# Performance work log

Measured on AMD Instinct MI355X. Metric: run time of the kernel, lower is better.

## Reference

```python
import jax, jax.numpy as jnp
import numpy as np

HID = 64
CTX = 64
STEPS = 2
RANK = 16
NODES = 1024
B, T = 16, 24
EPS = 1e-5


def _linear(x, W, b):
    # torch nn.Linear: x @ W.T + b, W is [out, in]
    return jnp.einsum('...i,oi->...o', x, W) + b


def _gelu(x):
    return jax.nn.gelu(x, approximate=False)


def _diffusion(adj, state, Ws, bs):
    # Ws: [S, out, in], bs: [S, out]
    term = jnp.zeros_like(state)
    for s in range(Ws.shape[0]):
        state = jnp.einsum('nm,btmf->btnf', adj, state)
        term = term + _linear(state, Ws[s], bs[s])
    return term


def setup_inputs() -> dict:
    key = jax.random.key(0)
    ks = jax.random.split(key, 32)
    f32 = jnp.float32
    def w(k, *shape, scale=None):
        s = scale if scale is not None else 1.0 / np.sqrt(shape[-1])
        return jax.random.uniform(k, shape, f32, -s, s)
    inp = {
        'x': jax.random.normal(ks[0], (B, T, NODES, HID), f32),
        'a_fwd': jax.random.uniform(ks[1], (NODES, NODES), f32),
        'context': jax.random.normal(ks[2], (B, T, NODES, CTX), f32),
        'W_self': w(ks[3], HID, HID), 'b_self': w(ks[4], HID),
        'W_fwd': w(ks[5], STEPS, HID, HID), 'b_fwd': w(ks[6], STEPS, HID),
        'W_bwd': w(ks[7], STEPS, HID, HID), 'b_bwd': w(ks[8], STEPS, HID),
        'W_adp': w(ks[9], STEPS, HID, HID), 'b_adp': w(ks[10], STEPS, HID),
        'Wg1': w(ks[11], HID, CTX), 'bg1': w(ks[12], HID),
        'Wg2': w(ks[13], 4, HID), 'bg2': w(ks[14], 4),
        'Ws1': w(ks[15], HID, CTX), 'bs1': w(ks[16], HID),
        'Ws2': w(ks[17], HID, HID), 'bs2': w(ks[18], HID),
        'W_src': w(ks[19], 1, CTX), 'b_src': w(ks[20], 1),
        'W_dst': w(ks[21], 1, CTX), 'b_dst': w(ks[22], 1),
        'emb_src': jax.random.normal(ks[23], (NODES, RANK), f32) * 0.02,
        'emb_dst': jax.random.normal(ks[24], (NODES, RANK), f32) * 0.02,
        'gamma': jnp.ones((HID,), f32), 'beta': jnp.zeros((HID,), f32),
    }
    return inp


def reference(x, a_fwd, context, W_self, b_self, W_fwd, b_fwd, W_bwd, b_bwd,
              W_adp, b_adp, Wg1, bg1, Wg2, bg2, Ws1, bs1, Ws2, bs2,
              W_src, b_src, W_dst, b_dst, emb_src, emb_dst, gamma, beta):
    a_bwd = a_fwd.T
    # adaptive adjacency: softmax(relu(Es @ Ed^T)) over last dim
    a_adp = jax.nn.softmax(jax.nn.relu(emb_src @ emb_dst.T), axis=-1)

    gates = jax.nn.sigmoid(_linear(_gelu(_linear(context, Wg1, bg1)), Wg2, bg2))  # [b,t,n,4]
    scale = jax.nn.sigmoid(_linear(_gelu(_linear(context, Ws1, bs1)), Ws2, bs2))  # [b,t,n,F]
    src_gate = jax.nn.sigmoid(_linear(context, W_src, b_src))  # [b,t,n,1]
    dst_gate = jax.nn.sigmoid(_linear(context, W_dst, b_dst))  # [b,t,n,1]

    self_term = _linear(x, W_self, b_self)
    fwd_term = _diffusion(a_fwd, x * dst_gate, W_fwd, b_fwd)
    bwd_term = _diffusion(a_bwd, x * src_gate, W_bwd, b_bwd)
    adp_term = _diffusion(a_adp, x, W_adp, b_adp)

    mixed = (gates[..., 0:1] * self_term + gates[..., 1:2] * fwd_term
             + gates[..., 2:3] * bwd_term + gates[..., 3:4] * adp_term) * scale

    h = x + _gelu(mixed)  # dropout is identity in eval mode
    mu = jnp.mean(h, axis=-1, keepdims=True)
    var = jnp.mean(jnp.square(h - mu), axis=-1, keepdims=True)
    return (h - mu) * jax.lax.rsqrt(var + EPS) * gamma + beta
```

## Files before the change

### kernel.cpp

```cpp
#include <hip/hip_runtime.h>
#include <math.h>

typedef unsigned short u16;
typedef short short8 __attribute__((ext_vector_type(8)));
typedef float f32x4 __attribute__((ext_vector_type(4)));

#define LN_EPS 1e-5f

__device__ __forceinline__ float gelu_exact(float x){
    return 0.5f * x * (1.0f + erff(x * 0.70710678118654752f));
}
__device__ __forceinline__ float sigmoidf_(float x){
    return 1.0f / (1.0f + __expf(-x));
}
__device__ __forceinline__ u16 f2bf(float f){
    unsigned u = __float_as_uint(f);
    u += 0x7fffu + ((u >> 16) & 1u);
    return (u16)(u >> 16);
}
__device__ __forceinline__ float b2f(u16 u){
    return __uint_as_float(((unsigned)u) << 16);
}

#define GLLDS(gp, lp) __builtin_amdgcn_global_load_lds( \
    (const __attribute__((address_space(1))) unsigned int*)(const void*)(gp), \
    (__attribute__((address_space(3))) unsigned int*)(void*)(lp), 16, 0, 0)

__global__ __launch_bounds__(256) void k_adp(const float* __restrict__ es,
                                             const float* __restrict__ ed,
                                             u16* __restrict__ aadp){
    __shared__ float srow[1024];
    __shared__ float s_es[16];
    __shared__ float sredm[4];
    __shared__ float sreds[4];
    const int n   = blockIdx.x;
    const int tid = threadIdx.x;
    const int wid = tid >> 6, lane = tid & 63;
    if (tid < 16) s_es[tid] = es[n*16 + tid];
    __syncthreads();
    float lmax = 0.0f;
    for (int m = tid; m < 1024; m += 256){
        const float* edm = ed + m*16;
        float z = 0.f;
        #pragma unroll
        for (int r = 0; r < 16; r++) z = fmaf(s_es[r], edm[r], z);
        z = fmaxf(z, 0.0f);
        srow[m] = z;
        lmax = fmaxf(lmax, z);
    }
    #pragma unroll
    for (int o = 32; o > 0; o >>= 1) lmax = fmaxf(lmax, __shfl_xor(lmax, o, 64));
    if (lane == 0) sredm[wid] = lmax;
    __syncthreads();
    const float tmax = fmaxf(fmaxf(sredm[0], sredm[1]), fmaxf(sredm[2], sredm[3]));
    float lsum = 0.f;
    for (int m = tid; m < 1024; m += 256){
        float e = expf(srow[m] - tmax);
        srow[m] = e;
        lsum += e;
    }
    #pragma unroll
    for (int o = 32; o > 0; o >>= 1) lsum += __shfl_xor(lsum, o, 64);
    if (lane == 0) sreds[wid] = lsum;
    __syncthreads();
    const float inv = 1.0f / (sreds[0] + sreds[1] + sreds[2] + sreds[3]);
    for (int m = tid; m < 1024; m += 256) aadp[(size_t)n*1024 + m] = f2bf(srow[m] * inv);
}

__global__ __launch_bounds__(256) void k_cvtbwd(const float* __restrict__ a,
                                                u16* __restrict__ afwd,
                                                u16* __restrict__ abwd){
    __shared__ float t[32][33];
    const int bx = blockIdx.x*32, by = blockIdx.y*32;
    const int tx = threadIdx.x & 31, ty = threadIdx.x >> 5;
    #pragma unroll
    for (int i = 0; i < 4; i++){
        const float v = a[(size_t)(by + ty + 8*i)*1024 + bx + tx];
        t[ty + 8*i][tx] = v;
        afwd[(size_t)(by + ty + 8*i)*1024 + bx + tx] = f2bf(v);
    }
    __syncthreads();
    #pragma unroll
    for (int i = 0; i < 4; i++)
        abwd[(size_t)(bx + ty + 8*i)*1024 + by + tx] = f2bf(t[tx][ty + 8*i]);
}

__global__ __launch_bounds__(256, 4) void k_gating(
    const float* __restrict__ x,    const float* __restrict__ ctx,
    const float* __restrict__ Wg1,  const float* __restrict__ bg1,
    const float* __restrict__ Wg2,  const float* __restrict__ bg2,
    const float* __restrict__ Ws1,  const float* __restrict__ bs1,
    const float* __restrict__ Ws2,  const float* __restrict__ bs2,
    const float* __restrict__ Wsrc, const float* __restrict__ bsrc,
    const float* __restrict__ Wdst, const float* __restrict__ bdst,
    const float* __restrict__ Wself,const float* __restrict__ bself,
    float* __restrict__ gates, u16* __restrict__ scaleb,
    float* __restrict__ acc,
    u16* __restrict__ xTp, u16* __restrict__ xTd, u16* __restrict__ xTs)
{
    __shared__ u16 H1[8192];
    __shared__ u16 H2[8192];
    __shared__ float sgate[128], dgate[128];

    const int tid  = threadIdx.x;
    const int wv   = tid >> 6, lane = tid & 63;
    const int lr   = lane & 15, lg = lane >> 4;
    const int wtok = wv * 32;
    const int tokbase = blockIdx.x * 128;
    const int bt = blockIdx.x >> 3;
    const int n0 = (blockIdx.x & 7) * 128;

    auto stage_coop = [&](u16* H, const float* g){
        #pragma unroll
        for (int i = 0; i < 8; i++){
            const int fid = i*256 + tid;
            const int t = fid >> 4, q = fid & 15;
            const float4 v = *(const float4*)&g[(size_t)t*64 + q*4];
            ushort4 s;
            s.x = f2bf(v.x); s.y = f2bf(v.y); s.z = f2bf(v.z); s.w = f2bf(v.w);
            *(ushort4*)&H[t*64 + ((((q>>1) ^ (t & 7)) << 3) | ((q & 1)*4))] = s;
        }
    };
    auto afrag = [&](const u16* H, int row, int kb)->short8{
        return *(const short8*)&H[wv*2048 + row*64 + ((kb ^ (row & 7)) << 3)];
    };
    auto wfrag = [&](const float* W, int o, int kb8)->short8{
        const float4 a = *(const float4*)&W[o*64 + kb8];
        const float4 b = *(const float4*)&W[o*64 + kb8 + 4];
        short8 s;
        s[0]=f2bf(a.x); s[1]=f2bf(a.y); s[2]=f2bf(a.z); s[3]=f2bf(a.w);
        s[4]=f2bf(b.x); s[5]=f2bf(b.y); s[6]=f2bf(b.z); s[7]=f2bf(b.w);
        return s;
    };
    auto gemm32 = [&](const u16* Hs, const float* W, const float* bias, f32x4 (&c)[2][4]){
        #pragma unroll
        for (int n = 0; n < 4; n++){
            const float bv = bias[n*16 + lr];
            #pragma unroll
            for (int m = 0; m < 2; m++){ f32x4 t = {bv,bv,bv,bv}; c[m][n] = t; }
        }
        #pragma unroll
        for (int kk = 0; kk < 2; kk++){
            short8 a[2];
            #pragma unroll
            for (int m = 0; m < 2; m++) a[m] = afrag(Hs, m*16 + lr, kk*4 + lg);
            #pragma unroll
            for (int n = 0; n < 4; n++){
                const short8 w = wfrag(W, n*16 + lr, kk*32 + lg*8);
                #pragma unroll
                for (int m = 0; m < 2; m++)
                    c[m][n] = __builtin_amdgcn_mfma_f32_16x16x32_bf16(a[m], w, c[m][n], 0,0,0);
            }
        }
    };
    auto storeH = [&](u16* Hd, f32x4 (&c)[2][4]){
        #pragma unroll
        for (int m = 0; m < 2; m++)
            #pragma unroll
            for (int n = 0; n < 4; n++){
                const int f = n*16 + lr;
                #pragma unroll
                for (int r = 0; r < 4; r++){
                    const int t = m*16 + lg*4 + r;
                    Hd[wv*2048 + t*64 + ((((f>>3) ^ (t & 7)) << 3) | (f & 7))] = f2bf(c[m][n][r]);
                }
            }
    };

    stage_coop(H1, ctx + (size_t)tokbase*64);
    __syncthreads();

    f32x4 c[2][4];

    gemm32(H1, Wg1, bg1, c);
    #pragma unroll
    for (int m = 0; m < 2; m++)
        #pragma unroll
        for (int n = 0; n < 4; n++)
            #pragma unroll
            for (int r = 0; r < 4; r++) c[m][n][r] = gelu_exact(c[m][n][r]);
    storeH(H2, c);

    {
        f32x4 c2[2];
        const float bv = (lr == 0) ? bsrc[0] : (lr == 1 ? bdst[0] : 0.f);
        #pragma unroll
        for (int m = 0; m < 2; m++){ f32x4 t = {bv,bv,bv,bv}; c2[m] = t; }
        #pragma unroll
        for (int kk = 0; kk < 2; kk++){
            short8 a[2];
            #pragma unroll
            for (int m = 0; m < 2; m++) a[m] = afrag(H1, m*16 + lr, kk*4 + lg);
            short8 w = {0,0,0,0,0,0,0,0};
            if (lr == 0) w = wfrag(Wsrc, 0, kk*32 + lg*8);
            else if (lr == 1) w = wfrag(Wdst, 0, kk*32 + lg*8);
            #pragma unroll
            for (int m = 0; m < 2; m++)
                c2[m] = __builtin_amdgcn_mfma_f32_16x16x32_bf16(a[m], w, c2[m], 0,0,0);
        }
        #pragma unroll
        for (int m = 0; m < 2; m++)
            #pragma unroll
            for (int r = 0; r < 4; r++){
                const int t = wtok + m*16 + lg*4 + r;
                const float v = sigmoidf_(c2[m][r]);
                if (lr == 0) sgate[t] = v;
                if (lr == 1) dgate[t] = v;
            }
    }

    gemm32(H1, Ws1, bs1, c);
    #pragma unroll
    for (int m = 0; m < 2; m++)
        #pragma unroll
        for (int n = 0; n < 4; n++)
            #pragma unroll
            for (int r = 0; r < 4; r++) c[m][n][r] = gelu_exact(c[m][n][r]);
    storeH(H1, c);

    float g0[2][4];
    {
        f32x4 c3[2];
        const float bv = (lr < 4) ? bg2[lr] : 0.f;
        #pragma unroll
        for (int m = 0; m < 2; m++){ f32x4 t = {bv,bv,bv,bv}; c3[m] = t; }
        #pragma unroll
        for (int kk = 0; kk < 2; kk++){
            short8 a[2];
            #pragma unroll
            for (int m = 0; m < 2; m++) a[m] = afrag(H2, m*16 + lr, kk*4 + lg);
            short8 w = {0,0,0,0,0,0,0,0};
            if (lr < 4) w = wfrag(Wg2, lr, kk*32 + lg*8);
            #pragma unroll
            for (int m = 0; m < 2; m++)
                c3[m] = __builtin_amdgcn_mfma_f32_16x16x32_bf16(a[m], w, c3[m], 0,0,0);
        }
        #pragma unroll
        for (int m = 0; m < 2; m++)
            #pragma unroll
            for (int r = 0; r < 4; r++){
                const float v = sigmoidf_(c3[m][r]);
                if (lr < 4)
                    gates[(size_t)(tokbase + wtok + m*16 + lg*4 + r)*4 + lr] = v;
                g0[m][r] = __shfl(v, lane & 48, 64);
            }
    }

    gemm32(H1, Ws2, bs2, c);
    #pragma unroll
    for (int m = 0; m < 2; m++)
        #pragma unroll
        for (int n = 0; n < 4; n++)
            #pragma unroll
            for (int r = 0; r < 4; r++) c[m][n][r] = sigmoidf_(c[m][n][r]);
    storeH(H1, c);
    {
        #pragma unroll
        for (int it = 0; it < 4; it++){
            const int r2  = wtok + it*8 + (lane >> 3);
            const int sub = lane & 7;
            const short8 v = *(const short8*)&H1[r2*64 + ((sub ^ (r2 & 7)) << 3)];
            *(short8*)&scaleb[(size_t)(tokbase + r2)*64 + sub*8] = v;
        }
    }

    __syncthreads();
    stage_coop(H2, x + (size_t)tokbase*64);
    __syncthreads();

    gemm32(H2, Wself, bself, c);
    #pragma unroll
    for (int m = 0; m < 2; m++)
        #pragma unroll
        for (int n = 0; n < 4; n++)
            #pragma unroll
            for (int r = 0; r < 4; r++)
                acc[(size_t)(tokbase + wtok + m*16 + lg*4 + r)*64 + n*16 + lr]
                    = g0[m][r] * c[m][n][r];

    {
        const int tok  = tid & 127;
        const int fbh  = tid >> 7;
        const float dg = dgate[tok], sg = sgate[tok];
        const size_t ob = (size_t)bt*65536 + n0 + tok;
        #pragma unroll
        for (int q = 0; q < 4; q++){
            const int fb = fbh*4 + q;
            const short8 v = *(const short8*)&H2[tok*64 + ((fb ^ (tok & 7)) << 3)];
            #pragma unroll
            for (int j = 0; j < 8; j++){
                const u16 raw = (u16)v[j];
                const float xv = b2f(raw);
                const size_t o = ob + (size_t)(fb*8 + j)*1024;
                xTp[o] = raw;
                xTd[o] = f2bf(xv * dg);
                xTs[o] = f2bf(xv * sg);
            }
        }
    }
}

template<bool WRITE_TMP, bool FINAL>
__global__ __launch_bounds__(256, 2) void k_diffmm(
    const u16* __restrict__ adj,  const u16* __restrict__ srcT,
    const float* __restrict__ W,  const float* __restrict__ bias,
    const float* __restrict__ gates, const int branch,
    float* __restrict__ acc, u16* __restrict__ tmpT,
    const float* __restrict__ x, const u16* __restrict__ scaleb,
    const float* __restrict__ gamma, const float* __restrict__ beta)
{
    __shared__ u16 sA[2][256*64];
    __shared__ u16 sB[2][64*64];

    const int tid = threadIdx.x;
    const int fb_ = blockIdx.x;
    const int s_  = (fb_ & 7) * 192 + (fb_ >> 3);
    const int bt  = s_ >> 2;
    const int n0  = (s_ & 3) * 256;
    const int wv  = tid >> 6, lane = tid & 63;
    const int lr  = lane & 15, lg = lane >> 4;
    const int wrow0 = wv * 64;

    const u16* asrc = adj  + (size_t)n0 * 1024;
    const u16* bsrc = srcT + (size_t)bt * 65536;

    auto stage = [&](int buf, int kt){
        const int m0 = kt * 64;
        #pragma unroll
        for (int i = 0; i < 8; i++){
            const int s = i*256 + tid;
            const int row = s >> 3, kbp = s & 7;
            const int kb = kbp ^ (row & 7);
            GLLDS(asrc + (size_t)row*1024 + m0 + kb*8, &sA[buf][s*8]);
        }
        #pragma unroll
        for (int i = 0; i < 2; i++){
            const int s = i*256 + tid;
            const int row = s >> 3, kbp = s & 7;
            const int kb = kbp ^ (row & 7);
            GLLDS(bsrc + (size_t)row*1024 + m0 + kb*8, &sB[buf][s*8]);
        }
    };

    const f32x4 z4 = {0.f, 0.f, 0.f, 0.f};
    f32x4 c[4][4];
    #pragma unroll
    for (int m = 0; m < 4; m++)
        #pragma unroll
        for (int n = 0; n < 4; n++) c[m][n] = z4;

    stage(0, 0);
    asm volatile("s_waitcnt vmcnt(0)" ::: "memory");
    __syncthreads();

    int cur = 0;
    for (int kt = 0; kt < 16; kt++){
        if (kt < 15) stage(cur ^ 1, kt + 1);
        const u16* A = sA[cur];
        const u16* B = sB[cur];
        short8 af[2][4], bfr[2][4];
        #pragma unroll
        for (int kk = 0; kk < 2; kk++){
            const int kb = lg + kk*4;
            #pragma unroll
            for (int m = 0; m < 4; m++){
                const int row = wrow0 + m*16 + lr;
                af[kk][m] = *(const short8*)&A[row*64 + ((kb ^ (row & 7)) << 3)];
            }
            #pragma unroll
            for (int n = 0; n < 4; n++){
                const int fr = n*16 + lr;
                bfr[kk][n] = *(const short8*)&B[fr*64 + ((kb ^ (fr & 7)) << 3)];
            }
        }
        #pragma unroll
        for (int kk = 0; kk < 2; kk++)
            #pragma unroll
            for (int m = 0; m < 4; m++)
                #pragma unroll
                for (int n = 0; n < 4; n++)
                    c[m][n] = __builtin_amdgcn_mfma_f32_16x16x32_bf16(
                        af[kk][m], bfr[kk][n], c[m][n], 0, 0, 0);
        asm volatile("s_waitcnt vmcnt(0)" ::: "memory");
        __syncthreads();
        cur ^= 1;
    }

    u16* yT = &sA[0][0];
    u16* sW = &sB[0][0];
    #pragma unroll
    for (int m = 0; m < 4; m++)
        #pragma unroll
        for (int n = 0; n < 4; n++){
            const int f = n*16 + lr;
            #pragma unroll
            for (int r = 0; r < 4; r++){
                const int row = wrow0 + m*16 + lg*4 + r;
                yT[row*64 + (((f >> 3) ^ (row & 7)) << 3) + (f & 7)] = f2bf(c[m][n][r]);
            }
        }
    for (int i = tid; i < 4096; i += 256){
        const int o = i >> 6, f = i & 63;
        sW[o*64 + (((f >> 3) ^ (o & 7)) << 3) + (f & 7)] = f2bf(W[i]);
    }
    __syncthreads();

    if (WRITE_TMP){
        const size_t ob = (size_t)bt*65536 + n0 + tid;
        #pragma unroll
        for (int fbk = 0; fbk < 8; fbk++){
            const short8 v = *(const short8*)&yT[tid*64 + ((fbk ^ (tid & 7)) << 3)];
            #pragma unroll
            for (int j = 0; j < 8; j++)
                tmpT[ob + (size_t)(fbk*8 + j)*1024] = (u16)v[j];
        }
    }

    f32x4 lin[4][4];
    #pragma unroll
    for (int m = 0; m < 4; m++)
        #pragma unroll
        for (int n = 0; n < 4; n++) lin[m][n] = z4;
    #pragma unroll
    for (int kk = 0; kk < 2; kk++){
        const int kb = lg + kk*4;
        short8 ya[4], wb[4];
        #pragma unroll
        for (int m = 0; m < 4; m++){
            const int row = wrow0 + m*16 + lr;
            ya[m] = *(const short8*)&yT[row*64 + ((kb ^ (row & 7)) << 3)];
        }
        #pragma unroll
        for (int n = 0; n < 4; n++){
            const int o = n*16 + lr;
            wb[n] = *(const short8*)&sW[o*64 + ((kb ^ (o & 7)) << 3)];
        }
        #pragma unroll
        for (int m = 0; m < 4; m++)
            #pragma unroll
            for (int n = 0; n < 4; n++)
                lin[m][n] = __builtin_amdgcn_mfma_f32_16x16x32_bf16(
                    ya[m], wb[n], lin[m][n], 0, 0, 0);
    }

    if constexpr (!FINAL){
        #pragma unroll
        for (int m = 0; m < 4; m++){
            float g[4];
            #pragma unroll
            for (int r = 0; r < 4; r++){
                const int node = n0 + wrow0 + m*16 + lg*4 + r;
                g[r] = gates[((size_t)bt*1024 + node)*4 + branch];
            }
            #pragma unroll
            for (int n = 0; n < 4; n++){
                const int f  = n*16 + lr;
                const float bv = bias[f];
                #pragma unroll
                for (int r = 0; r < 4; r++){
                    const int node = n0 + wrow0 + m*16 + lg*4 + r;
                    float* p = &acc[((size_t)bt*1024 + node)*64 + f];
                    *p += g[r] * (lin[m][n][r] + bv);
                }
            }
        }
    } else {
        #pragma unroll
        for (int m = 0; m < 4; m++){
            #pragma unroll
            for (int r = 0; r < 4; r++){
                const int node = n0 + wrow0 + m*16 + lg*4 + r;
                const size_t tok = (size_t)bt*1024 + node;
                const float g = gates[tok*4 + branch];
                float h[4];
                #pragma unroll
                for (int n = 0; n < 4; n++){
                    const int f = n*16 + lr;
                    const float a = acc[tok*64 + f] + g * (lin[m][n][r] + bias[f]);
                    const float mixed = a * b2f(scaleb[tok*64 + f]);
                    h[n] = x[tok*64 + f] + gelu_exact(mixed);
                }
                float s = h[0] + h[1] + h[2] + h[3];
                #pragma unroll
                for (int o = 8; o > 0; o >>= 1) s += __shfl_xor(s, o, 64);
                const float mu = s * (1.0f/64.0f);
                float vs = 0.f;
                #pragma unroll
                for (int n = 0; n < 4; n++){ const float d = h[n] - mu; vs += d*d; }
                #pragma unroll
                for (int o = 8; o > 0; o >>= 1) vs += __shfl_xor(vs, o, 64);
                const float inv = rsqrtf(vs * (1.0f/64.0f) + LN_EPS);
                #pragma unroll
                for (int n = 0; n < 4; n++){
                    const int f = n*16 + lr;
                    acc[tok*64 + f] = (h[n] - mu) * inv * gamma[f] + beta[f];
                }
            }
        }
    }
}

extern "C" void kernel_launch(void* const* d_in, const int* in_sizes, int n_in,
                              void* d_out, int out_size, void* d_ws, size_t ws_size,
                              hipStream_t stream)
{
    const float* x      = (const float*)d_in[0];
    const float* a_fwd  = (const float*)d_in[1];
    const float* ctx    = (const float*)d_in[2];
    const float* W_self = (const float*)d_in[3];
    const float* b_self = (const float*)d_in[4];
    const float* W_fwd  = (const float*)d_in[5];
    const float* b_fwd  = (const float*)d_in[6];
    const float* W_bwd  = (const float*)d_in[7];
    const float* b_bwd  = (const float*)d_in[8];
    const float* W_adp  = (const float*)d_in[9];
    const float* b_adp  = (const float*)d_in[10];
    const float* Wg1    = (const float*)d_in[11];
    const float* bg1    = (const float*)d_in[12];
    const float* Wg2    = (const float*)d_in[13];
    const float* bg2    = (const float*)d_in[14];
    const float* Ws1    = (const float*)d_in[15];
    const float* bs1    = (const float*)d_in[16];
    const float* Ws2    = (const float*)d_in[17];
    const float* bs2    = (const float*)d_in[18];
    const float* W_src  = (const float*)d_in[19];
    const float* b_src  = (const float*)d_in[20];
    const float* W_dst  = (const float*)d_in[21];
    const float* b_dst  = (const float*)d_in[22];
    const float* emb_src= (const float*)d_in[23];
    const float* emb_dst= (const float*)d_in[24];
    const float* gamma  = (const float*)d_in[25];
    const float* beta   = (const float*)d_in[26];

    float* out = (float*)d_out;
    char*  w   = (char*)d_ws;
    const size_t MB48 = 50331648ull;
    u16* afwd_bf = (u16*)(w);
    u16* abwd_bf = (u16*)(w + 2097152ull);
    u16* aadp_bf = (u16*)(w + 4194304ull);
    u16* xTp     = (u16*)(w + 6291456ull);
    u16* xTd     = (u16*)(w + 6291456ull + 1*MB48);
    u16* xTs     = (u16*)(w + 6291456ull + 2*MB48);
    u16* tmpT    = (u16*)(w + 6291456ull + 3*MB48);
    u16* scaleb  = (u16*)(w + 6291456ull + 4*MB48);
    float* gates = (float*)(w + 6291456ull + 5*MB48);

    k_adp   <<<1024, 256, 0, stream>>>(emb_src, emb_dst, aadp_bf);
    k_cvtbwd<<<dim3(32,32), 256, 0, stream>>>(a_fwd, afwd_bf, abwd_bf);
    k_gating<<<3072, 256, 0, stream>>>(x, ctx, Wg1,bg1, Wg2,bg2, Ws1,bs1, Ws2,bs2,
                                       W_src,b_src, W_dst,b_dst, W_self,b_self,
                                       gates, scaleb, out, xTp, xTd, xTs);

    k_diffmm<true ,false><<<1536,256,0,stream>>>(afwd_bf, xTd,  W_fwd,      b_fwd,
                                                 gates, 1, out, tmpT,
                                                 nullptr, nullptr, nullptr, nullptr);
    k_diffmm<false,false><<<1536,256,0,stream>>>(afwd_bf, tmpT, W_fwd+4096, b_fwd+64,
                                                 gates, 1, out, nullptr,
                                                 nullptr, nullptr, nullptr, nullptr);
    k_diffmm<true ,false><<<1536,256,0,stream>>>(abwd_bf, xTs,  W_bwd,      b_bwd,
                                                 gates, 2, out, tmpT,
                                                 nullptr, nullptr, nullptr, nullptr);
    k_diffmm<false,false><<<1536,256,0,stream>>>(abwd_bf, tmpT, W_bwd+4096, b_bwd+64,
                                                 gates, 2, out, nullptr,
                                                 nullptr, nullptr, nullptr, nullptr);
    k_diffmm<true ,false><<<1536,256,0,stream>>>(aadp_bf, xTp,  W_adp,      b_adp,
                                                 gates, 3, out, tmpT,
                                                 nullptr, nullptr, nullptr, nullptr);
    k_diffmm<false,true ><<<1536,256,0,stream>>>(aadp_bf, tmpT, W_adp+4096, b_adp+64,
                                                 gates, 3, out, nullptr,
                                                 x, scaleb, gamma, beta);
}
```

Before: 1.053 ms.

## Store branch accumulator in bf16 and pre-convert all weights once

Adds a prep kernel that converts every linear weight to bf16 once, so the gating and diffusion kernels read bf16 weight fragments straight from global memory instead of converting floats in each block. The running accumulator across the gated branches moves from fp32 in the output buffer to a separate bf16 workspace. Diffusion kernels stage their contributions in LDS and then do vectorized read-modify-write of that accumulator. The aim is to halve accumulator traffic and remove per-block weight conversion. The cost is extra bf16 rounding on every accumulation step, which may hurt accuracy.

```diff
diff --git a/kernel.cpp b/kernel.cpp
--- a/kernel.cpp
+++ b/kernel.cpp
@@ -25,6 +25,30 @@
 #define GLLDS(gp, lp) __builtin_amdgcn_global_load_lds( \
     (const __attribute__((address_space(1))) unsigned int*)(const void*)(gp), \
     (__attribute__((address_space(3))) unsigned int*)(void*)(lp), 16, 0, 0)
+
+__global__ __launch_bounds__(256) void k_prep(
+    const float* __restrict__ Wg1, const float* __restrict__ Ws1,
+    const float* __restrict__ Ws2, const float* __restrict__ Wself,
+    const float* __restrict__ Wg2, const float* __restrict__ Wsrc,
+    const float* __restrict__ Wdst, const float* __restrict__ Wfwd,
+    const float* __restrict__ Wbwd, const float* __restrict__ Wadp,
+    u16* __restrict__ wbf)
+{
+    const int i = blockIdx.x*256 + threadIdx.x;
+    if (i >= 41344) return;
+    const float* src; int off;
+    if      (i < 4096)  { src = Wg1;  off = 0; }
+    else if (i < 8192)  { src = Ws1;  off = 4096; }
+    else if (i < 12288) { src = Ws2;  off = 8192; }
+    else if (i < 16384) { src = Wself;off = 12288; }
+    else if (i < 24576) { src = Wfwd; off = 16384; }
+    else if (i < 32768) { src = Wbwd; off = 24576; }
+    else if (i < 40960) { src = Wadp; off = 32768; }
+    else if (i < 41216) { src = Wg2;  off = 40960; }
+    else if (i < 41280) { src = Wsrc; off = 41216; }
+    else                { src = Wdst; off = 41280; }
+    wbf[i] = f2bf(src[i - off]);
+}
 
 __global__ __launch_bounds__(256) void k_adp(const float* __restrict__ es,
                                              const float* __restrict__ ed,
@@ -87,15 +111,15 @@
 
 __global__ __launch_bounds__(256, 4) void k_gating(
     const float* __restrict__ x,    const float* __restrict__ ctx,
-    const float* __restrict__ Wg1,  const float* __restrict__ bg1,
-    const float* __restrict__ Wg2,  const float* __restrict__ bg2,
-    const float* __restrict__ Ws1,  const float* __restrict__ bs1,
-    const float* __restrict__ Ws2,  const float* __restrict__ bs2,
-    const float* __restrict__ Wsrc, const float* __restrict__ bsrc,
-    const float* __restrict__ Wdst, const float* __restrict__ bdst,
-    const float* __restrict__ Wself,const float* __restrict__ bself,
+    const u16* __restrict__ wg1,  const float* __restrict__ bg1,
+    const u16* __restrict__ wg2,  const float* __restrict__ bg2,
+    const u16* __restrict__ ws1,  const float* __restrict__ bs1,
+    const u16* __restrict__ ws2,  const float* __restrict__ bs2,
+    const u16* __restrict__ wsrc, const float* __restrict__ bsrc,
+    const u16* __restrict__ wdst, const float* __restrict__ bdst,
+    const u16* __restrict__ wself,const float* __restrict__ bself,
     float* __restrict__ gates, u16* __restrict__ scaleb,
-    float* __restrict__ acc,
+    u16* __restrict__ accb,
     u16* __restrict__ xTp, u16* __restrict__ xTd, u16* __restrict__ xTs)
 {
     __shared__ u16 H1[8192];
@@ -124,15 +148,10 @@
     auto afrag = [&](const u16* H, int row, int kb)->short8{
         return *(const short8*)&H[wv*2048 + row*64 + ((kb ^ (row & 7)) << 3)];
     };
-    auto wfrag = [&](const float* W, int o, int kb8)->short8{
-        const float4 a = *(const float4*)&W[o*64 + kb8];
-        const float4 b = *(const float4*)&W[o*64 + kb8 + 4];
-        short8 s;
-        s[0]=f2bf(a.x); s[1]=f2bf(a.y); s[2]=f2bf(a.z); s[3]=f2bf(a.w);
-        s[4]=f2bf(b.x); s[5]=f2bf(b.y); s[6]=f2bf(b.z); s[7]=f2bf(b.w);
-        return s;
+    auto wfrag = [&](const u16* W, int o, int kb8)->short8{
+        return *(const short8*)&W[o*64 + kb8];
     };
-    auto gemm32 = [&](const u16* Hs, const float* W, const float* bias, f32x4 (&c)[2][4]){
+    auto gemm32 = [&](const u16* Hs, const u16* W, const float* bias, f32x4 (&c)[2][4]){
         #pragma unroll
         for (int n = 0; n < 4; n++){
             const float bv = bias[n*16 + lr];
@@ -172,7 +191,7 @@
 
     f32x4 c[2][4];
 
-    gemm32(H1, Wg1, bg1, c);
+    gemm32(H1, wg1, bg1, c);
     #pragma unroll
     for (int m = 0; m < 2; m++)
         #pragma unroll
@@ -192,8 +211,8 @@
             #pragma unroll
             for (int m = 0; m < 2; m++) a[m] = afrag(H1, m*16 + lr, kk*4 + lg);
             short8 w = {0,0,0,0,0,0,0,0};
-            if (lr == 0) w = wfrag(Wsrc, 0, kk*32 + lg*8);
-            else if (lr == 1) w = wfrag(Wdst, 0, kk*32 + lg*8);
+            if (lr == 0) w = wfrag(wsrc, 0, kk*32 + lg*8);
+            else if (lr == 1) w = wfrag(wdst, 0, kk*32 + lg*8);
             #pragma unroll
             for (int m = 0; m < 2; m++)
                 c2[m] = __builtin_amdgcn_mfma_f32_16x16x32_bf16(a[m], w, c2[m], 0,0,0);
@@ -209,7 +228,7 @@
             }
     }
 
-    gemm32(H1, Ws1, bs1, c);
+    gemm32(H1, ws1, bs1, c);
     #pragma unroll
     for (int m = 0; m < 2; m++)
         #pragma unroll
@@ -230,7 +249,7 @@
             #pragma unroll
             for (int m = 0; m < 2; m++) a[m] = afrag(H2, m*16 + lr, kk*4 + lg);
             short8 w = {0,0,0,0,0,0,0,0};
-            if (lr < 4) w = wfrag(Wg2, lr, kk*32 + lg*8);
+            if (lr < 4) w = wfrag(wg2, lr, kk*32 + lg*8);
             #pragma unroll
             for (int m = 0; m < 2; m++)
                 c3[m] = __builtin_amdgcn_mfma_f32_16x16x32_bf16(a[m], w, c3[m], 0,0,0);
@@ -246,7 +265,7 @@
             }
     }
 
-    gemm32(H1, Ws2, bs2, c);
+    gemm32(H1, ws2, bs2, c);
     #pragma unroll
     for (int m = 0; m < 2; m++)
         #pragma unroll
@@ -268,15 +287,23 @@
     stage_coop(H2, x + (size_t)tokbase*64);
     __syncthreads();
 
-    gemm32(H2, Wself, bself, c);
+    gemm32(H2, wself, bself, c);
     #pragma unroll
     for (int m = 0; m < 2; m++)
         #pragma unroll
         for (int n = 0; n < 4; n++)
             #pragma unroll
-            for (int r = 0; r < 4; r++)
-                acc[(size_t)(tokbase + wtok + m*16 + lg*4 + r)*64 + n*16 + lr]
-                    = g0[m][r] * c[m][n][r];
+            for (int r = 0; r < 4; r++) c[m][n][r] *= g0[m][r];
+    storeH(H1, c);
+    {
+        #pragma unroll
+        for (int it = 0; it < 4; it++){
+            const int r2  = wtok + it*8 + (lane >> 3);
+            const int sub = lane & 7;
+            const short8 v = *(const short8*)&H1[r2*64 + ((sub ^ (r2 & 7)) << 3)];
+            *(short8*)&accb[(size_t)(tokbase + r2)*64 + sub*8] = v;
+        }
+    }
 
     {
         const int tok  = tid & 127;
@@ -303,11 +330,12 @@
 template<bool WRITE_TMP, bool FINAL>
 __global__ __launch_bounds__(256, 2) void k_diffmm(
     const u16* __restrict__ adj,  const u16* __restrict__ srcT,
-    const float* __restrict__ W,  const float* __restrict__ bias,
+    const u16* __restrict__ Wbf,  const float* __restrict__ bias,
     const float* __restrict__ gates, const int branch,
-    float* __restrict__ acc, u16* __restrict__ tmpT,
+    u16* __restrict__ accb, u16* __restrict__ tmpT,
     const float* __restrict__ x, const u16* __restrict__ scaleb,
-    const float* __restrict__ gamma, const float* __restrict__ beta)
+    const float* __restrict__ gamma, const float* __restrict__ beta,
+    float* __restrict__ out)
 {
     __shared__ u16 sA[2][256*64];
     __shared__ u16 sB[2][64*64];
@@ -387,7 +415,7 @@
     }
 
     u16* yT = &sA[0][0];
-    u16* sW = &sB[0][0];
+    u16* eL = &sA[1][0];
     #pragma unroll
     for (int m = 0; m < 4; m++)
         #pragma unroll
@@ -399,10 +427,6 @@
                 yT[row*64 + (((f >> 3) ^ (row & 7)) << 3) + (f & 7)] = f2bf(c[m][n][r]);
             }
         }
-    for (int i = tid; i < 4096; i += 256){
-        const int o = i >> 6, f = i & 63;
-        sW[o*64 + (((f >> 3) ^ (o & 7)) << 3) + (f & 7)] = f2bf(W[i]);
-    }
     __syncthreads();
 
     if (WRITE_TMP){
@@ -431,10 +455,8 @@
             ya[m] = *(const short8*)&yT[row*64 + ((kb ^ (row & 7)) << 3)];
         }
         #pragma unroll
-        for (int n = 0; n < 4; n++){
-            const int o = n*16 + lr;
-            wb[n] = *(const short8*)&sW[o*64 + ((kb ^ (o & 7)) << 3)];
-        }
+        for (int n = 0; n < 4; n++)
+            wb[n] = *(const short8*)&Wbf[(n*16 + lr)*64 + kb*8];
         #pragma unroll
         for (int m = 0; m < 4; m++)
             #pragma unroll
@@ -454,15 +476,27 @@
             }
             #pragma unroll
             for (int n = 0; n < 4; n++){
-                const int f  = n*16 + lr;
+                const int f = n*16 + lr;
                 const float bv = bias[f];
                 #pragma unroll
                 for (int r = 0; r < 4; r++){
-                    const int node = n0 + wrow0 + m*16 + lg*4 + r;
-                    float* p = &acc[((size_t)bt*1024 + node)*64 + f];
-                    *p += g[r] * (lin[m][n][r] + bv);
+                    const int row = wrow0 + m*16 + lg*4 + r;
+                    eL[row*64 + (((f >> 3) ^ (row & 7)) << 3) + (f & 7)]
+                        = f2bf(g[r] * (lin[m][n][r] + bv));
                 }
             }
+        }
+        __syncthreads();
+        const size_t tokb = ((size_t)bt*1024 + n0 + tid)*64;
+        #pragma unroll
+        for (int fbk = 0; fbk < 8; fbk++){
+            const short8 e = *(const short8*)&eL[tid*64 + ((fbk ^ (tid & 7)) << 3)];
+            const short8 a = *(const short8*)&accb[tokb + fbk*8];
+            short8 o;
+            #pragma unroll
+            for (int j = 0; j < 8; j++)
+                o[j] = (short)f2bf(b2f((u16)a[j]) + b2f((u16)e[j]));
+            *(short8*)&accb[tokb + fbk*8] = o;
         }
     } else {
         #pragma unroll
@@ -476,7 +510,7 @@
                 #pragma unroll
                 for (int n = 0; n < 4; n++){
                     const int f = n*16 + lr;
-                    const float a = acc[tok*64 + f] + g * (lin[m][n][r] + bias[f]);
+                    const float a = b2f(accb[tok*64 + f]) + g * (lin[m][n][r] + bias[f]);
                     const float mixed = a * b2f(scaleb[tok*64 + f]);
                     h[n] = x[tok*64 + f] + gelu_exact(mixed);
                 }
@@ -493,7 +527,7 @@
                 #pragma unroll
                 for (int n = 0; n < 4; n++){
                     const int f = n*16 + lr;
-                    acc[tok*64 + f] = (h[n] - mu) * inv * gamma[f] + beta[f];
+                    out[tok*64 + f] = (h[n] - mu) * inv * gamma[f] + beta[f];
                 }
             }
         }
@@ -543,30 +577,37 @@
     u16* xTs     = (u16*)(w + 6291456ull + 2*MB48);
     u16* tmpT    = (u16*)(w + 6291456ull + 3*MB48);
     u16* scaleb  = (u16*)(w + 6291456ull + 4*MB48);
-    float* gates = (float*)(w + 6291456ull + 5*MB48);
-
+    u16* accb    = (u16*)(w + 6291456ull + 5*MB48);
+    float* gates = (float*)(w + 6291456ull + 6*MB48);
+    u16* wbf     = (u16*)(w + 6291456ull + 6*MB48 + 8388608ull);
+
+    k_prep  <<<162, 256, 0, stream>>>(Wg1, Ws1, Ws2, W_self, Wg2, W_src, W_dst,
+                                      W_fwd, W_bwd, W_adp, wbf);
     k_adp   <<<1024, 256, 0, stream>>>(emb_src, emb_dst, aadp_bf);
     k_cvtbwd<<<dim3(32,32), 256, 0, stream>>>(a_fwd, afwd_bf, abwd_bf);
-    k_gating<<<3072, 256, 0, stream>>>(x, ctx, Wg1,bg1, Wg2,bg2, Ws1,bs1, Ws2,bs2,
-                                       W_src,b_src, W_dst,b_dst, W_self,b_self,
-                                       gates, scaleb, out, xTp, xTd, xTs);
-
-    k_diffmm<true ,false><<<1536,256,0,stream>>>(afwd_bf, xTd,  W_fwd,      b_fwd,
-                                                 gates, 1, out, tmpT,
-                                                 nullptr, nullptr, nullptr, nullptr);
-    k_diffmm<false,false><<<1536,256,0,stream>>>(afwd_bf, tmpT, W_fwd+4096, b_fwd+64,
-                                                 gates, 1, out, nullptr,
-                                                 nullptr, nullptr, nullptr, nullptr);
-    k_diffmm<true ,false><<<1536,256,0,stream>>>(abwd_bf, xTs,  W_bwd,      b_bwd,
-                                                 gates, 2, out, tmpT,
-                                                 nullptr, nullptr, nullptr, nullptr);
-    k_diffmm<false,false><<<1536,256,0,stream>>>(abwd_bf, tmpT, W_bwd+4096, b_bwd+64,
-                                                 gates, 2, out, nullptr,
-                                                 nullptr, nullptr, nullptr, nullptr);
-    k_diffmm<true ,false><<<1536,256,0,stream>>>(aadp_bf, xTp,  W_adp,      b_adp,
-                                                 gates, 3, out, tmpT,
-                                                 nullptr, nullptr, nullptr, nullptr);
-    k_diffmm<false,true ><<<1536,256,0,stream>>>(aadp_bf, tmpT, W_adp+4096, b_adp+64,
-                                                 gates, 3, out, nullptr,
-                                                 x, scaleb, gamma, beta);
-}
+    k_gating<<<3072, 256, 0, stream>>>(x, ctx,
+                                       wbf + 0,     bg1,  wbf + 40960, bg2,
+                                       wbf + 4096,  bs1,  wbf + 8192,  bs2,
+                                       wbf + 41216, b_src, wbf + 41280, b_dst,
+                                       wbf + 12288, b_self,
+                                       gates, scaleb, accb, xTp, xTd, xTs);
+
+    k_diffmm<true ,false><<<1536,256,0,stream>>>(afwd_bf, xTd,  wbf+16384, b_fwd,
+                                                 gates, 1, accb, tmpT,
+                                                 nullptr, nullptr, nullptr, nullptr, nullptr);
+    k_diffmm<false,false><<<1536,256,0,stream>>>(afwd_bf, tmpT, wbf+20480, b_fwd+64,
+                                                 gates, 1, accb, nullptr,
+                                                 nullptr, nullptr, nullptr, nullptr, nullptr);
+    k_diffmm<true ,false><<<1536,256,0,stream>>>(abwd_bf, xTs,  wbf+24576, b_bwd,
+                                                 gates, 2, accb, tmpT,
+                                                 nullptr, nullptr, nullptr, nullptr, nullptr);
+    k_diffmm<false,false><<<1536,256,0,stream>>>(abwd_bf, tmpT, wbf+28672, b_bwd+64,
+                                                 gates, 2, accb, nullptr,
+                                                 nullptr, nullptr, nullptr, nullptr, nullptr);
+    k_diffmm<true ,false><<<1536,256,0,stream>>>(aadp_bf, xTp,  wbf+32768, b_adp,
+                                                 gates, 3, accb, tmpT,
+                                                 nullptr, nullptr, nullptr, nullptr, nullptr);
+    k_diffmm<false,true ><<<1536,256,0,stream>>>(aadp_bf, tmpT, wbf+36864, b_adp+64,
+                                                 gates, 3, accb, nullptr,
+                                                 x, scaleb, gamma, beta, out);
+}
```

After: 986.0 us. 6.3% less time.
